# Performance work log

Hardware: AMD Instinct MI355X
Metric: run time of the kernel (lower is better)

The kernel has to match this reference:

```python
import jax, jax.numpy as jnp
import numpy as np

B, S, H = 4, 2048, 1024
E, I, K = 8, 2048, 2


def setup_inputs() -> dict:
    key = jax.random.key(0)
    ks = jax.random.split(key, 6)
    return {
        "hidden_states": jax.random.normal(ks[0], (B, S, H), dtype=jnp.float32),
        "Wg": jax.random.normal(ks[1], (H, E), dtype=jnp.float32) * 0.02,
        "W1": jax.random.normal(ks[2], (E, H, I), dtype=jnp.float32) * 0.02,
        "b1": jnp.zeros((E, I), dtype=jnp.float32),
        "W2": jax.random.normal(ks[3], (E, I, H), dtype=jnp.float32) * 0.02,
        "b2": jnp.zeros((E, H), dtype=jnp.float32),
    }


def reference(hidden_states, Wg, W1, b1, W2, b2):
    b, s, h = hidden_states.shape
    x = hidden_states.reshape(-1, h)                      # [T, H]
    gate_logits = x @ Wg                                  # [T, E]
    gate_probs = jax.nn.softmax(gate_logits, axis=-1)
    topk_probs, topk_idx = jax.lax.top_k(gate_probs, K)   # [T, K]
    topk_probs = topk_probs / jnp.sum(topk_probs, axis=-1, keepdims=True)
    # dense combine weights [T, E] (zero where expert not selected)
    T = x.shape[0]
    w = jnp.zeros((T, E), dtype=x.dtype)
    w = w.at[jnp.arange(T)[:, None], topk_idx].set(topk_probs)
    # run every expert on all tokens (dense grouped-GEMM form), exact erf GELU
    h1 = jax.nn.gelu(jnp.einsum('th,ehi->eti', x, W1) + b1[:, None, :], approximate=False)  # [E, T, I]
    y = jnp.einsum('eti,eih->eth', h1, W2) + b2[:, None, :]                                  # [E, T, H]
    out = jnp.einsum('te,eth->th', w, y)                                                     # [T, H]
    return out.reshape(b, s, h)
```

## Files before the change

kernel.cpp:

```cpp
#include <hip/hip_runtime.h>
#include <math.h>

#define TOKS 8192
#define HD 1024
#define ID 2048
#define NE 8

typedef __bf16 bf16_t;
typedef __bf16 bf16x8 __attribute__((ext_vector_type(8)));
typedef float f32x4 __attribute__((ext_vector_type(4)));

#define GLOAD(gp, lp)                                                \
  __builtin_amdgcn_global_load_lds(                                  \
      (const __attribute__((address_space(1))) void*)(gp),           \
      (__attribute__((address_space(3))) void*)(lp), 16, 0, 0)

#define WAITV(N) asm volatile("s_waitcnt vmcnt(" #N ")" ::: "memory")
#define WAITL0() asm volatile("s_waitcnt lgkmcnt(0)" ::: "memory")

__device__ __forceinline__ float gelu_exact(float v) {
  const float u = v * 0.70710678118654752f;
  const float a = fabsf(u);
  const float t = 1.f / (1.f + 0.3275911f * a);
  const float poly =
      t * (0.254829592f +
           t * (-0.284496736f +
                t * (1.421413741f + t * (-1.453152027f + t * 1.061405429f))));
  float er = 1.f - poly * __expf(-a * a);
  er = copysignf(er, u);
  return 0.5f * v * (1.f + er);
}

#define WS_COUNTS 0
#define WS_OFFSETS 32
#define WS_BTOK 128
#define WS_BW (128 + 65536)
#define WS_TE (128 + 2 * 65536)
#define WS_TW (128 + 3 * 65536)
#define WS_WL 263168ull
#define WS_POS 274432ull
#define WS_RANK 339968ull
#define WS_BLKC 405504ull
#define WS_BLKB 438272ull
#define WS_XB 524288ull
#define WS_H1 (WS_XB + 16777216ull)
#define WS_WT (WS_H1 + 67108864ull)
#define WS_Y (WS_WT + 33554432ull)

#define MAXWL 144
#define BM 128
#define GB (TOKS / 8)

__global__ __launch_bounds__(256) void gate_kernel(const float* __restrict__ x,
                                                   const float* __restrict__ Wg,
                                                   bf16_t* __restrict__ xb,
                                                   int* __restrict__ tok_e,
                                                   float* __restrict__ tok_w,
                                                   int* __restrict__ rank_of,
                                                   int* __restrict__ blk_cnt) {
  __shared__ float WgT[HD * NE];
  __shared__ int cnt[NE];
  const int tid = threadIdx.x;
#pragma unroll
  for (int i = 0; i < NE * HD / (256 * 4); ++i) {
    const int k = i * 256 + tid;
    ((float4*)WgT)[k] = ((const float4*)Wg)[k];
  }
  if (tid < NE) cnt[tid] = 0;
  __syncthreads();
  const int wv = tid >> 6;
  const int lane = tid & 63;
#pragma unroll
  for (int s = 0; s < 2; ++s) {
    const int t = blockIdx.x * 8 + wv * 2 + s;
    const float* xrow = x + (size_t)t * HD;
    bf16_t* xbrow = xb + (size_t)t * HD;
    float acc[NE];
#pragma unroll
    for (int e = 0; e < NE; ++e) acc[e] = 0.f;
#pragma unroll
    for (int i = 0; i < 16; ++i) {
      const int h = i * 64 + lane;
      const float xv = xrow[h];
      xbrow[h] = (bf16_t)xv;
      const float4 w0 = *(const float4*)(WgT + h * NE);
      const float4 w1 = *(const float4*)(WgT + h * NE + 4);
      acc[0] += xv * w0.x;
      acc[1] += xv * w0.y;
      acc[2] += xv * w0.z;
      acc[3] += xv * w0.w;
      acc[4] += xv * w1.x;
      acc[5] += xv * w1.y;
      acc[6] += xv * w1.z;
      acc[7] += xv * w1.w;
    }
#pragma unroll
    for (int off = 32; off >= 1; off >>= 1) {
#pragma unroll
      for (int e = 0; e < NE; ++e) acc[e] += __shfl_xor(acc[e], off);
    }
    if (lane == 0) {
      int i1 = 0;
      float l1 = acc[0];
#pragma unroll
      for (int e = 1; e < NE; ++e)
        if (acc[e] > l1) { l1 = acc[e]; i1 = e; }
      int i2 = -1;
      float l2 = -3.4e38f;
#pragma unroll
      for (int e = 0; e < NE; ++e)
        if (e != i1 && acc[e] > l2) { l2 = acc[e]; i2 = e; }
      const float q = expf(l2 - l1);
      const float w1 = 1.f / (1.f + q);
      tok_e[2 * t] = i1;
      tok_e[2 * t + 1] = i2;
      tok_w[2 * t] = w1;
      tok_w[2 * t + 1] = q * w1;
      rank_of[2 * t] = atomicAdd(&cnt[i1], 1);
      rank_of[2 * t + 1] = atomicAdd(&cnt[i2], 1);
    }
  }
  __syncthreads();
  if (tid < NE) blk_cnt[blockIdx.x * NE + tid] = cnt[tid];
}

__global__ void scan_kernel(const int* __restrict__ blk_cnt, int* __restrict__ counts,
                            int* __restrict__ offsets, int* __restrict__ blk_base,
                            int* __restrict__ wl_e, int* __restrict__ wl_m,
                            int* __restrict__ n_work) {
  const int b = threadIdx.x;
  int sum[NE], pre[NE], tot[NE];
#pragma unroll
  for (int e = 0; e < NE; ++e) {
    int s = 0;
    for (int j = 0; j < 16; ++j) s += blk_cnt[(b * 16 + j) * NE + e];
    sum[e] = s;
  }
#pragma unroll
  for (int e = 0; e < NE; ++e) {
    int v = sum[e];
#pragma unroll
    for (int off = 1; off < 64; off <<= 1) {
      const int u = __shfl_up(v, off);
      if (b >= off) v += u;
    }
    pre[e] = v - sum[e];
    tot[e] = __shfl(v, 63);
  }
  int off_[NE];
  int s = 0;
#pragma unroll
  for (int e = 0; e < NE; ++e) {
    off_[e] = s;
    s += tot[e];
  }
#pragma unroll
  for (int e = 0; e < NE; ++e) {
    int run = off_[e] + pre[e];
    for (int j = 0; j < 16; ++j) {
      blk_base[(b * 16 + j) * NE + e] = run;
      run += blk_cnt[(b * 16 + j) * NE + e];
    }
  }
  if (b == 0) {
    int idx = 0;
    for (int e = 0; e < NE; ++e) {
      counts[e] = tot[e];
      offsets[e] = off_[e];
      for (int m = 0; m < tot[e] && idx < MAXWL; m += BM) {
        wl_e[idx] = e;
        wl_m[idx] = m;
        ++idx;
      }
    }
    *n_work = idx;
  }
}

__global__ __launch_bounds__(256) void scatter_kernel(const int* __restrict__ tok_e,
                                                      const float* __restrict__ tok_w,
                                                      const int* __restrict__ blk_base,
                                                      const int* __restrict__ rank_of,
                                                      int* __restrict__ bucket_tok,
                                                      float* __restrict__ bucket_w,
                                                      int* __restrict__ pos_of) {
  const int idx = blockIdx.x * 256 + threadIdx.x;
  const int e = tok_e[idx];
  const int gb = idx >> 4;
  const int pos = blk_base[gb * NE + e] + rank_of[idx];
  bucket_tok[pos] = idx >> 1;
  bucket_w[pos] = tok_w[idx];
  pos_of[idx] = pos;
}

__global__ __launch_bounds__(256) void transpose_convert_kernel(const float* __restrict__ src,
                                                                bf16_t* __restrict__ dst, int K,
                                                                int N) {
  __shared__ float tile[64][65];
  const int e = blockIdx.z;
  const int k0 = blockIdx.x * 64;
  const int n0 = blockIdx.y * 64;
  const float* s = src + (size_t)e * K * N;
  bf16_t* d = dst + (size_t)e * K * N;
  const int t = threadIdx.x;
  const int c4 = (t & 15) * 4;
  const int rr = t >> 4;
#pragma unroll
  for (int p = 0; p < 4; ++p) {
    const int r = p * 16 + rr;
    const float4 v = *(const float4*)(s + (size_t)(k0 + r) * N + n0 + c4);
    tile[r][c4] = v.x;
    tile[r][c4 + 1] = v.y;
    tile[r][c4 + 2] = v.z;
    tile[r][c4 + 3] = v.w;
  }
  __syncthreads();
  const int kc = t & 7;
  const int nb = t >> 3;
#pragma unroll
  for (int p = 0; p < 2; ++p) {
    const int n = p * 32 + nb;
    bf16_t o[8];
#pragma unroll
    for (int j = 0; j < 8; ++j) o[j] = (bf16_t)tile[kc * 8 + j][n];
    *(uint4*)(d + (size_t)(n0 + n) * K + k0 + kc * 8) = *(uint4*)o;
  }
}


__global__ __launch_bounds__(256, 3) void gemm1_kernel(
    const bf16_t* __restrict__ xb, const bf16_t* __restrict__ W1T, const float* __restrict__ b1,
    const int* __restrict__ counts, const int* __restrict__ offsets,
    const int* __restrict__ bucket_tok, const int* __restrict__ wl_e,
    const int* __restrict__ wl_m, const int* __restrict__ n_work, bf16_t* __restrict__ h1) {
  const int widx = blockIdx.x;
  if (widx >= *n_work) return;
  const int e = wl_e[widx];
  const int m_base = wl_m[widx];
  const int n_e = counts[e];
  const int n_base = blockIdx.y * 128;
  const int off = offsets[e];

  __shared__ bf16_t As[3][128 * 32];
  __shared__ bf16_t Bs[3][128 * 32];

  const int tid = threadIdx.x;
  const int w = tid >> 6;
  const int lane = tid & 63;
  const int quad = lane >> 4;
  const int lrow = lane & 15;
  const int wm = w >> 1;
  const int wn = w & 1;

  const int srow = lane >> 2;
  const int kch = (((lane & 3) ^ ((lane >> 4) & 3)) * 8);
  int r0 = m_base + w * 32 + srow;
  int r1 = r0 + 16;
  if (r0 >= n_e) r0 = n_e - 1;
  if (r1 >= n_e) r1 = n_e - 1;
  const bf16_t* ga0 = xb + (size_t)bucket_tok[off + r0] * HD + kch;
  const bf16_t* ga1 = xb + (size_t)bucket_tok[off + r1] * HD + kch;
  const bf16_t* gb0 = W1T + ((size_t)e * ID + n_base + w * 32 + srow) * HD + kch;
  const bf16_t* gb1 = gb0 + (size_t)16 * HD;
  const int laofs0 = w * 1024 + lane * 8;
  const int laofs1 = laofs0 + 512;

  f32x4 acc[4][4];
#pragma unroll
  for (int mt = 0; mt < 4; ++mt)
#pragma unroll
    for (int nt = 0; nt < 4; ++nt)
#pragma unroll
      for (int r = 0; r < 4; ++r) acc[mt][nt][r] = 0.f;

#pragma unroll
  for (int p = 0; p < 2; ++p) {
    const size_t ko = (size_t)p * 32;
    GLOAD(ga0 + ko, &As[p][laofs0]);
    GLOAD(ga1 + ko, &As[p][laofs1]);
    GLOAD(gb0 + ko, &Bs[p][laofs0]);
    GLOAD(gb1 + ko, &Bs[p][laofs1]);
  }

  const int slot = (quad ^ ((lrow >> 2) & 3)) * 8;
  int cur = 0;
  int pre = 2;
#define NT1 (HD / 32)
  for (int kt = 0; kt < NT1; ++kt) {
    WAITL0();
    __builtin_amdgcn_s_barrier();
    if (kt + 2 < NT1) {
      const size_t ko = (size_t)(kt + 2) * 32;
      GLOAD(ga0 + ko, &As[pre][laofs0]);
      GLOAD(ga1 + ko, &As[pre][laofs1]);
      GLOAD(gb0 + ko, &Bs[pre][laofs0]);
      GLOAD(gb1 + ko, &Bs[pre][laofs1]);
      WAITV(8);
    } else if (kt + 1 < NT1) {
      WAITV(4);
    } else {
      WAITV(0);
    }
    __builtin_amdgcn_s_barrier();
    __builtin_amdgcn_sched_barrier(0);
    bf16x8 af[4], bfr[4];
#pragma unroll
    for (int i = 0; i < 4; ++i) {
      af[i] = *(const bf16x8*)(&As[cur][(wm * 64 + i * 16 + lrow) * 32 + slot]);
      bfr[i] = *(const bf16x8*)(&Bs[cur][(wn * 64 + i * 16 + lrow) * 32 + slot]);
    }
    __builtin_amdgcn_s_setprio(1);
#pragma unroll
    for (int mt = 0; mt < 4; ++mt)
#pragma unroll
      for (int nt = 0; nt < 4; ++nt)
        acc[mt][nt] =
            __builtin_amdgcn_mfma_f32_16x16x32_bf16(bfr[nt], af[mt], acc[mt][nt], 0, 0, 0);
    __builtin_amdgcn_s_setprio(0);
    cur = (cur == 2) ? 0 : cur + 1;
    pre = (pre == 2) ? 0 : pre + 1;
  }

#pragma unroll
  for (int mt = 0; mt < 4; ++mt) {
    const int gm = m_base + wm * 64 + mt * 16 + lrow;
    if (gm < n_e) {
      bf16_t* orow = h1 + (size_t)(off + gm) * ID;
#pragma unroll
      for (int nt = 0; nt < 4; ++nt) {
        const int gi0 = n_base + wn * 64 + nt * 16 + quad * 4;
        const float4 bb = *(const float4*)(b1 + e * ID + gi0);
        const float bv[4] = {bb.x, bb.y, bb.z, bb.w};
        bf16_t o[4];
#pragma unroll
        for (int r = 0; r < 4; ++r) o[r] = (bf16_t)gelu_exact(acc[mt][nt][r] + bv[r]);
        *(uint2*)(orow + gi0) = *(uint2*)o;
      }
    }
  }
}

__global__ __launch_bounds__(256, 3) void gemm2_kernel(
    const bf16_t* __restrict__ h1, const bf16_t* __restrict__ W2T, const float* __restrict__ b2,
    const int* __restrict__ counts, const int* __restrict__ offsets,
    const int* __restrict__ wl_e, const int* __restrict__ wl_m, const int* __restrict__ n_work,
    bf16_t* __restrict__ y) {
  const int widx = blockIdx.x;
  if (widx >= *n_work) return;
  const int e = wl_e[widx];
  const int m_base = wl_m[widx];
  const int n_e = counts[e];
  const int n_base = blockIdx.y * 128;
  const int off = offsets[e];

  __shared__ bf16_t As[3][128 * 32];
  __shared__ bf16_t Bs[3][128 * 32];

  const int tid = threadIdx.x;
  const int w = tid >> 6;
  const int lane = tid & 63;
  const int quad = lane >> 4;
  const int lrow = lane & 15;
  const int wm = w >> 1;
  const int wn = w & 1;

  const int srow = lane >> 2;
  const int kch = (((lane & 3) ^ ((lane >> 4) & 3)) * 8);
  int r0 = m_base + w * 32 + srow;
  int r1 = r0 + 16;
  if (r0 >= n_e) r0 = n_e - 1;
  if (r1 >= n_e) r1 = n_e - 1;
  const bf16_t* ga0 = h1 + (size_t)(off + r0) * ID + kch;
  const bf16_t* ga1 = h1 + (size_t)(off + r1) * ID + kch;
  const bf16_t* gb0 = W2T + ((size_t)e * HD + n_base + w * 32 + srow) * ID + kch;
  const bf16_t* gb1 = gb0 + (size_t)16 * ID;
  const int laofs0 = w * 1024 + lane * 8;
  const int laofs1 = laofs0 + 512;

  f32x4 acc[4][4];
#pragma unroll
  for (int mt = 0; mt < 4; ++mt)
#pragma unroll
    for (int nt = 0; nt < 4; ++nt)
#pragma unroll
      for (int r = 0; r < 4; ++r) acc[mt][nt][r] = 0.f;

#pragma unroll
  for (int p = 0; p < 2; ++p) {
    const size_t ko = (size_t)p * 32;
    GLOAD(ga0 + ko, &As[p][laofs0]);
    GLOAD(ga1 + ko, &As[p][laofs1]);
    GLOAD(gb0 + ko, &Bs[p][laofs0]);
    GLOAD(gb1 + ko, &Bs[p][laofs1]);
  }

  const int slot = (quad ^ ((lrow >> 2) & 3)) * 8;
  int cur = 0;
  int pre = 2;
#define NT2 (ID / 32)
  for (int kt = 0; kt < NT2; ++kt) {
    WAITL0();
    __builtin_amdgcn_s_barrier();
    if (kt + 2 < NT2) {
      const size_t ko = (size_t)(kt + 2) * 32;
      GLOAD(ga0 + ko, &As[pre][laofs0]);
      GLOAD(ga1 + ko, &As[pre][laofs1]);
      GLOAD(gb0 + ko, &Bs[pre][laofs0]);
      GLOAD(gb1 + ko, &Bs[pre][laofs1]);
      WAITV(8);
    } else if (kt + 1 < NT2) {
      WAITV(4);
    } else {
      WAITV(0);
    }
    __builtin_amdgcn_s_barrier();
    __builtin_amdgcn_sched_barrier(0);
    bf16x8 af[4], bfr[4];
#pragma unroll
    for (int i = 0; i < 4; ++i) {
      af[i] = *(const bf16x8*)(&As[cur][(wm * 64 + i * 16 + lrow) * 32 + slot]);
      bfr[i] = *(const bf16x8*)(&Bs[cur][(wn * 64 + i * 16 + lrow) * 32 + slot]);
    }
    __builtin_amdgcn_s_setprio(1);
#pragma unroll
    for (int mt = 0; mt < 4; ++mt)
#pragma unroll
      for (int nt = 0; nt < 4; ++nt)
        acc[mt][nt] =
            __builtin_amdgcn_mfma_f32_16x16x32_bf16(bfr[nt], af[mt], acc[mt][nt], 0, 0, 0);
    __builtin_amdgcn_s_setprio(0);
    cur = (cur == 2) ? 0 : cur + 1;
    pre = (pre == 2) ? 0 : pre + 1;
  }

#pragma unroll
  for (int mt = 0; mt < 4; ++mt) {
    const int gm = m_base + wm * 64 + mt * 16 + lrow;
    if (gm < n_e) {
      bf16_t* orow = y + (size_t)(off + gm) * HD;
#pragma unroll
      for (int nt = 0; nt < 4; ++nt) {
        const int gi0 = n_base + wn * 64 + nt * 16 + quad * 4;
        const float4 bb = *(const float4*)(b2 + e * HD + gi0);
        const float bv[4] = {bb.x, bb.y, bb.z, bb.w};
        bf16_t o[4];
#pragma unroll
        for (int r = 0; r < 4; ++r) o[r] = (bf16_t)(acc[mt][nt][r] + bv[r]);
        *(uint2*)(orow + gi0) = *(uint2*)o;
      }
    }
  }
}

__global__ __launch_bounds__(256) void combine_kernel(const bf16_t* __restrict__ y,
                                                      const int* __restrict__ pos_of,
                                                      const float* __restrict__ tok_w,
                                                      float* __restrict__ out) {
  const int gid = blockIdx.x * 256 + threadIdx.x;
  const int t = gid >> 7;
  const int c8 = (gid & 127) * 8;
  const int p1 = pos_of[2 * t];
  const int p2 = pos_of[2 * t + 1];
  const float w1 = tok_w[2 * t];
  const float w2 = tok_w[2 * t + 1];
  const bf16x8 a = *(const bf16x8*)(y + (size_t)p1 * HD + c8);
  const bf16x8 b = *(const bf16x8*)(y + (size_t)p2 * HD + c8);
  float* op = out + (size_t)t * HD + c8;
  float ov[8];
#pragma unroll
  for (int j = 0; j < 8; ++j) ov[j] = w1 * (float)a[j] + w2 * (float)b[j];
  *(float4*)op = make_float4(ov[0], ov[1], ov[2], ov[3]);
  *(float4*)(op + 4) = make_float4(ov[4], ov[5], ov[6], ov[7]);
}

extern "C" void kernel_launch(void* const* d_in, const int* in_sizes, int n_in,
                              void* d_out, int out_size, void* d_ws, size_t ws_size,
                              hipStream_t stream) {
  const float* x = (const float*)d_in[0];
  const float* Wg = (const float*)d_in[1];
  const float* W1 = (const float*)d_in[2];
  const float* b1 = (const float*)d_in[3];
  const float* W2 = (const float*)d_in[4];
  const float* b2 = (const float*)d_in[5];
  float* out = (float*)d_out;
  char* ws = (char*)d_ws;

  int* counts = (int*)(ws + WS_COUNTS);
  int* offsets = (int*)(ws + WS_OFFSETS);
  int* bucket_tok = (int*)(ws + WS_BTOK);
  float* bucket_w = (float*)(ws + WS_BW);
  int* tok_e = (int*)(ws + WS_TE);
  float* tok_w = (float*)(ws + WS_TW);
  int* wl_e = (int*)(ws + WS_WL);
  int* wl_m = wl_e + MAXWL;
  int* n_work = wl_m + MAXWL;
  int* pos_of = (int*)(ws + WS_POS);
  int* rank_of = (int*)(ws + WS_RANK);
  int* blk_cnt = (int*)(ws + WS_BLKC);
  int* blk_base = (int*)(ws + WS_BLKB);
  bf16_t* xb = (bf16_t*)(ws + WS_XB);
  bf16_t* h1 = (bf16_t*)(ws + WS_H1);
  bf16_t* WT = (bf16_t*)(ws + WS_WT);
  bf16_t* y = (bf16_t*)(ws + WS_Y);

  gate_kernel<<<GB, 256, 0, stream>>>(x, Wg, xb, tok_e, tok_w, rank_of, blk_cnt);
  scan_kernel<<<1, 64, 0, stream>>>(blk_cnt, counts, offsets, blk_base, wl_e, wl_m, n_work);
  scatter_kernel<<<TOKS * 2 / 256, 256, 0, stream>>>(tok_e, tok_w, blk_base, rank_of,
                                                     bucket_tok, bucket_w, pos_of);
  transpose_convert_kernel<<<dim3(HD / 64, ID / 64, NE), 256, 0, stream>>>(W1, WT, HD, ID);
  gemm1_kernel<<<dim3(MAXWL, ID / 128), 256, 0, stream>>>(xb, WT, b1, counts, offsets, bucket_tok,
                                                          wl_e, wl_m, n_work, h1);
  transpose_convert_kernel<<<dim3(ID / 64, HD / 64, NE), 256, 0, stream>>>(W2, WT, ID, HD);
  gemm2_kernel<<<dim3(MAXWL, HD / 128), 256, 0, stream>>>(h1, WT, b2, counts, offsets, wl_e,
                                                          wl_m, n_work, y);
  combine_kernel<<<TOKS * HD / (256 * 8), 256, 0, stream>>>(y, pos_of, tok_w, out);
}
```

Baseline: 447.4 us.

## Switch GEMM pipelines to double-buffered LDS and raise occupancy bound

Both grouped GEMM kernels move from a three-stage LDS ring with hand-placed vmcnt/lgkmcnt waits and split barriers to a simpler two-stage double buffer synchronized by __syncthreads. LDS per block drops from 48KB to 32KB, and the launch bound rises from 3 to 5 blocks per CU so more blocks can be resident to hide latency. In exchange the prefetch distance shrinks to one tile, and each iteration likely drains outstanding loads at the barrier. The tighter register budget, roughly 102 VGPRs for a kernel holding 64 accumulator and 32 fragment registers, risks spilling.

```diff
diff --git a/kernel.cpp b/kernel.cpp
--- a/kernel.cpp
+++ b/kernel.cpp
@@ -14,9 +14,6 @@
   __builtin_amdgcn_global_load_lds(                                  \
       (const __attribute__((address_space(1))) void*)(gp),           \
       (__attribute__((address_space(3))) void*)(lp), 16, 0, 0)
-
-#define WAITV(N) asm volatile("s_waitcnt vmcnt(" #N ")" ::: "memory")
-#define WAITL0() asm volatile("s_waitcnt lgkmcnt(0)" ::: "memory")
 
 __device__ __forceinline__ float gelu_exact(float v) {
   const float u = v * 0.70710678118654752f;
@@ -228,7 +225,7 @@
 }
 
 
-__global__ __launch_bounds__(256, 3) void gemm1_kernel(
+__global__ __launch_bounds__(256, 5) void gemm1_kernel(
     const bf16_t* __restrict__ xb, const bf16_t* __restrict__ W1T, const float* __restrict__ b1,
     const int* __restrict__ counts, const int* __restrict__ offsets,
     const int* __restrict__ bucket_tok, const int* __restrict__ wl_e,
@@ -241,8 +238,8 @@
   const int n_base = blockIdx.y * 128;
   const int off = offsets[e];
 
-  __shared__ bf16_t As[3][128 * 32];
-  __shared__ bf16_t Bs[3][128 * 32];
+  __shared__ bf16_t As[2][128 * 32];
+  __shared__ bf16_t Bs[2][128 * 32];
 
   const int tid = threadIdx.x;
   const int w = tid >> 6;
@@ -273,36 +270,24 @@
 #pragma unroll
       for (int r = 0; r < 4; ++r) acc[mt][nt][r] = 0.f;
 
-#pragma unroll
-  for (int p = 0; p < 2; ++p) {
-    const size_t ko = (size_t)p * 32;
-    GLOAD(ga0 + ko, &As[p][laofs0]);
-    GLOAD(ga1 + ko, &As[p][laofs1]);
-    GLOAD(gb0 + ko, &Bs[p][laofs0]);
-    GLOAD(gb1 + ko, &Bs[p][laofs1]);
-  }
+  GLOAD(ga0, &As[0][laofs0]);
+  GLOAD(ga1, &As[0][laofs1]);
+  GLOAD(gb0, &Bs[0][laofs0]);
+  GLOAD(gb1, &Bs[0][laofs1]);
+  __syncthreads();
 
   const int slot = (quad ^ ((lrow >> 2) & 3)) * 8;
-  int cur = 0;
-  int pre = 2;
 #define NT1 (HD / 32)
   for (int kt = 0; kt < NT1; ++kt) {
-    WAITL0();
-    __builtin_amdgcn_s_barrier();
-    if (kt + 2 < NT1) {
-      const size_t ko = (size_t)(kt + 2) * 32;
-      GLOAD(ga0 + ko, &As[pre][laofs0]);
-      GLOAD(ga1 + ko, &As[pre][laofs1]);
-      GLOAD(gb0 + ko, &Bs[pre][laofs0]);
-      GLOAD(gb1 + ko, &Bs[pre][laofs1]);
-      WAITV(8);
-    } else if (kt + 1 < NT1) {
-      WAITV(4);
-    } else {
-      WAITV(0);
-    }
-    __builtin_amdgcn_s_barrier();
-    __builtin_amdgcn_sched_barrier(0);
+    const int cur = kt & 1;
+    if (kt + 1 < NT1) {
+      const int nxt = cur ^ 1;
+      const size_t ko = (size_t)(kt + 1) * 32;
+      GLOAD(ga0 + ko, &As[nxt][laofs0]);
+      GLOAD(ga1 + ko, &As[nxt][laofs1]);
+      GLOAD(gb0 + ko, &Bs[nxt][laofs0]);
+      GLOAD(gb1 + ko, &Bs[nxt][laofs1]);
+    }
     bf16x8 af[4], bfr[4];
 #pragma unroll
     for (int i = 0; i < 4; ++i) {
@@ -317,8 +302,7 @@
         acc[mt][nt] =
             __builtin_amdgcn_mfma_f32_16x16x32_bf16(bfr[nt], af[mt], acc[mt][nt], 0, 0, 0);
     __builtin_amdgcn_s_setprio(0);
-    cur = (cur == 2) ? 0 : cur + 1;
-    pre = (pre == 2) ? 0 : pre + 1;
+    __syncthreads();
   }
 
 #pragma unroll
@@ -340,7 +324,7 @@
   }
 }
 
-__global__ __launch_bounds__(256, 3) void gemm2_kernel(
+__global__ __launch_bounds__(256, 5) void gemm2_kernel(
     const bf16_t* __restrict__ h1, const bf16_t* __restrict__ W2T, const float* __restrict__ b2,
     const int* __restrict__ counts, const int* __restrict__ offsets,
     const int* __restrict__ wl_e, const int* __restrict__ wl_m, const int* __restrict__ n_work,
@@ -353,8 +337,8 @@
   const int n_base = blockIdx.y * 128;
   const int off = offsets[e];
 
-  __shared__ bf16_t As[3][128 * 32];
-  __shared__ bf16_t Bs[3][128 * 32];
+  __shared__ bf16_t As[2][128 * 32];
+  __shared__ bf16_t Bs[2][128 * 32];
 
   const int tid = threadIdx.x;
   const int w = tid >> 6;
@@ -385,36 +369,24 @@
 #pragma unroll
       for (int r = 0; r < 4; ++r) acc[mt][nt][r] = 0.f;
 
-#pragma unroll
-  for (int p = 0; p < 2; ++p) {
-    const size_t ko = (size_t)p * 32;
-    GLOAD(ga0 + ko, &As[p][laofs0]);
-    GLOAD(ga1 + ko, &As[p][laofs1]);
-    GLOAD(gb0 + ko, &Bs[p][laofs0]);
-    GLOAD(gb1 + ko, &Bs[p][laofs1]);
-  }
+  GLOAD(ga0, &As[0][laofs0]);
+  GLOAD(ga1, &As[0][laofs1]);
+  GLOAD(gb0, &Bs[0][laofs0]);
+  GLOAD(gb1, &Bs[0][laofs1]);
+  __syncthreads();
 
   const int slot = (quad ^ ((lrow >> 2) & 3)) * 8;
-  int cur = 0;
-  int pre = 2;
 #define NT2 (ID / 32)
   for (int kt = 0; kt < NT2; ++kt) {
-    WAITL0();
-    __builtin_amdgcn_s_barrier();
-    if (kt + 2 < NT2) {
-      const size_t ko = (size_t)(kt + 2) * 32;
-      GLOAD(ga0 + ko, &As[pre][laofs0]);
-      GLOAD(ga1 + ko, &As[pre][laofs1]);
-      GLOAD(gb0 + ko, &Bs[pre][laofs0]);
-      GLOAD(gb1 + ko, &Bs[pre][laofs1]);
-      WAITV(8);
-    } else if (kt + 1 < NT2) {
-      WAITV(4);
-    } else {
-      WAITV(0);
-    }
-    __builtin_amdgcn_s_barrier();
-    __builtin_amdgcn_sched_barrier(0);
+    const int cur = kt & 1;
+    if (kt + 1 < NT2) {
+      const int nxt = cur ^ 1;
+      const size_t ko = (size_t)(kt + 1) * 32;
+      GLOAD(ga0 + ko, &As[nxt][laofs0]);
+      GLOAD(ga1 + ko, &As[nxt][laofs1]);
+      GLOAD(gb0 + ko, &Bs[nxt][laofs0]);
+      GLOAD(gb1 + ko, &Bs[nxt][laofs1]);
+    }
     bf16x8 af[4], bfr[4];
 #pragma unroll
     for (int i = 0; i < 4; ++i) {
@@ -429,8 +401,7 @@
         acc[mt][nt] =
             __builtin_amdgcn_mfma_f32_16x16x32_bf16(bfr[nt], af[mt], acc[mt][nt], 0, 0, 0);
     __builtin_amdgcn_s_setprio(0);
-    cur = (cur == 2) ? 0 : cur + 1;
-    pre = (pre == 2) ? 0 : pre + 1;
+    __syncthreads();
   }
 
 #pragma unroll
```

New measurement: 843.8 us. 1.89x slower.
